# Performance work log

Measured on AMD Instinct MI355X. Metric: run time of the kernel, lower is better.

## Reference

```python
import jax, jax.numpy as jnp
import numpy as np

NUM_SYMBOLS = 5
NUM_SUBCARRIERS = 33


def _dft_matrix(n):
    # Unitary DFT matrix: F[j,k] = exp(-2i*pi*j*k/n) / sqrt(n)
    omega = np.exp(-2j * np.pi / n)
    j, k = np.meshgrid(np.arange(n), np.arange(n))
    return (np.power(omega, j * k) / np.sqrt(n)).astype(np.complex64)


def setup_inputs() -> dict:
    key = jax.random.key(0)
    k1, k2 = jax.random.split(key)
    shape = (4096, NUM_SYMBOLS, 4, 4, NUM_SUBCARRIERS)  # (N, S, TXH, TXW, W)
    x_real = jax.random.normal(k1, shape, dtype=jnp.float32)
    x_imag = jax.random.normal(k2, shape, dtype=jnp.float32)
    F_sym = _dft_matrix(NUM_SYMBOLS)
    F_sub = _dft_matrix(NUM_SUBCARRIERS)
    return {
        "x_real": x_real,
        "x_imag": x_imag,
        "F_sym_real": jnp.asarray(F_sym.real, dtype=jnp.float32),
        "F_sym_imag": jnp.asarray(F_sym.imag, dtype=jnp.float32),
        "F_sub_real": jnp.asarray(F_sub.real, dtype=jnp.float32),
        "F_sub_imag": jnp.asarray(F_sub.imag, dtype=jnp.float32),
    }


def reference(x_real, x_imag, F_sym_real, F_sym_imag, F_sub_real, F_sub_imag):
    N, S, TXH, TXW, W = x_real.shape
    x = jax.lax.complex(x_real, x_imag).reshape(N, S, TXH * TXW, W)
    x = jnp.transpose(x, (0, 2, 1, 3))  # (N, A, S, W), A = TXH*TXW

    F_sym = jax.lax.complex(F_sym_real, F_sym_imag)  # (S, S)
    F_sub = jax.lax.complex(F_sub_real, F_sub_imag)  # (W, W)

    # 2D DFT across symbols (left) and subcarriers (right)
    X = jnp.einsum("st,natw->nasw", F_sym, x)
    X = jnp.einsum("nasw,wv->nasv", X, F_sub)

    # magnitude-square (power spectrum)
    X_mag_sq = (X.real * X.real + X.imag * X.imag).astype(jnp.complex64)

    # inverse 2D DFT (conjugate transposes) -> autocorrelation
    X = jnp.einsum("st,natw->nasw", F_sym.conj().T, X_mag_sq)
    X = jnp.einsum("nasw,wv->nasv", X, F_sub.conj().T)

    X = jnp.transpose(X, (0, 2, 1, 3))  # (N, S, A, W)
    return X.reshape(N, S, TXH, TXW, W)
```

## Files before the change

### kernel.cpp

```cpp
#include <hip/hip_runtime.h>

#define NS 5
#define NW 33
#define NA 16
#define SW 165
#define BUFS 99
#define CW 11
#define CH (CW*NS)
#define CE (CH*MPW)
#define MPW 5
#define GM 20
#define TPM 11
#define CPT 3
#define THREADS 256

typedef float f2 __attribute__((ext_vector_type(2)));

__device__ __forceinline__ void cmac(f2& z, f2 x, f2 f) {
    asm("v_pk_fma_f32 %0, %1, %2, %0 op_sel:[0,0,0] op_sel_hi:[1,0,1]"
        : "+v"(z) : "v"(x), "v"(f));
    asm("v_pk_fma_f32 %0, %1, %2, %0 op_sel:[1,1,0] op_sel_hi:[0,1,1] neg_lo:[1,0,0]"
        : "+v"(z) : "v"(x), "v"(f));
}

__device__ __forceinline__ void cmacr(f2& z, f2 f, f2 Pp) {
    asm("v_pk_fma_f32 %0, %1, %2, %0 op_sel:[0,0,0] op_sel_hi:[1,1,1] neg_hi:[1,0,0]"
        : "+v"(z) : "v"(f), "v"(Pp));
}

__device__ __forceinline__ void pkfma(f2& z, f2 a, f2 b) {
    asm("v_pk_fma_f32 %0, %1, %2, %0 op_sel:[0,0,0] op_sel_hi:[1,1,1]"
        : "+v"(z) : "v"(a), "v"(b));
}

#define STAGE_LOAD(R, W0)                                                  \
    _Pragma("unroll")                                                      \
    for (int i = 0; i < 5; ++i) {                                          \
        const int e = lane + i * 64;                                       \
        f2 v = (f2){0.f, 0.f};                                             \
        if (e < CE) {                                                      \
            const int gq = e / CH, rq = e - gq * CH;                       \
            const int tq = rq / CW, wq = rq - tq * CW;                     \
            const int Mq = Mw + gq;                                        \
            if (Mq < NM) {                                                 \
                const int nq = Mq >> 4, aq = Mq & 15;                      \
                const int go = ((nq * NS + tq) * NA + aq) * NW + (W0) + wq;\
                v = (f2){x_real[go], x_imag[go]};                          \
            }                                                              \
        }                                                                  \
        R[i] = v;                                                          \
    }

#define STAGE_WRITE(R)                                                     \
    _Pragma("unroll")                                                      \
    for (int i = 0; i < 5; ++i) {                                          \
        const int e = lane + i * 64;                                       \
        if (e < CE) {                                                      \
            const int gq = e / CH, rq = e - gq * CH;                       \
            const int tq = rq / CW, wq = rq - tq * CW;                     \
            wbuf[gq * BUFS + wq * NS + tq] = R[i];                         \
        }                                                                  \
    }

#define COMPUTE_CHUNK(W0)                                                  \
    if (act) {                                                             \
        const f2* bp = wbuf + gg * BUFS;                                   \
        _Pragma("unroll 3")                                                \
        for (int w = 0; w < CW; ++w) {                                     \
            f2 xc[NS];                                                     \
            _Pragma("unroll")                                              \
            for (int t = 0; t < NS; ++t) xc[t] = bp[w * NS + t];           \
            f2 fv[CPT];                                                    \
            _Pragma("unroll")                                              \
            for (int k = 0; k < CPT; ++k)                                  \
                fv[k] = sFsub[((W0) + w) * NW + c0 + k];                   \
            _Pragma("unroll")                                              \
            for (int t = 0; t < NS; ++t)                                   \
                _Pragma("unroll")                                          \
                for (int k = 0; k < CPT; ++k)                              \
                    cmac(V[t][k], xc[t], fv[k]);                           \
        }                                                                  \
    }

__global__ __launch_bounds__(THREADS, 6) void autocorr_kernel(
    const float* __restrict__ x_real, const float* __restrict__ x_imag,
    const float* __restrict__ Fsym_re, const float* __restrict__ Fsym_im,
    const float* __restrict__ Fsub_re, const float* __restrict__ Fsub_im,
    float* __restrict__ out, int NM, int write_complex)
{
    __shared__ f2 sFsym[NS * NS];
    __shared__ f2 sFsub[NW * NW];
    __shared__ f2 buf[GM * BUFS];

    const int tid = threadIdx.x;
    const int wave = tid >> 6;
    const int lane = tid & 63;
    const int Mw = blockIdx.x * GM + wave * MPW;
    f2* const wbuf = &buf[wave * MPW * BUFS];

    for (int i = tid; i < NW * NW; i += THREADS)
        sFsub[i] = (f2){Fsub_re[i], Fsub_im[i]};
    if (tid < NS * NS) sFsym[tid] = (f2){Fsym_re[tid], Fsym_im[tid]};

    f2 rA[5], rB[5];
    STAGE_LOAD(rA, 0);
    STAGE_WRITE(rA);
    __syncthreads();

    STAGE_LOAD(rB, CW);

    const int g = lane / TPM;
    const int j = lane - g * TPM;
    const bool act = (lane < MPW * TPM);
    const int gg = act ? g : 0;
    const int M = Mw + gg;
    const int Ms = (M < NM) ? M : 0;
    const int n = Ms >> 4, a = Ms & 15;
    const int c0 = 3 * j;

    f2 V[NS][CPT];
#pragma unroll
    for (int t = 0; t < NS; ++t)
#pragma unroll
        for (int k = 0; k < CPT; ++k) V[t][k] = (f2){0.f, 0.f};

    COMPUTE_CHUNK(0);
    STAGE_WRITE(rB);
    STAGE_LOAD(rA, 2 * CW);
    asm volatile("s_waitcnt lgkmcnt(0)" ::: "memory");
    COMPUTE_CHUNK(CW);
    STAGE_WRITE(rA);
    asm volatile("s_waitcnt lgkmcnt(0)" ::: "memory");
    COMPUTE_CHUNK(2 * CW);

    f2 T2[3][CPT];
#pragma unroll
    for (int p = 0; p < 3; ++p)
#pragma unroll
        for (int k = 0; k < CPT; ++k) T2[p][k] = (f2){0.f, 0.f};
    if (act) {
#pragma unroll
        for (int s = 0; s < NS; ++s) {
            f2 X[CPT];
#pragma unroll
            for (int k = 0; k < CPT; ++k) X[k] = (f2){0.f, 0.f};
#pragma unroll
            for (int t = 0; t < NS; ++t) {
                f2 f = sFsym[s * NS + t];
#pragma unroll
                for (int k = 0; k < CPT; ++k)
                    cmac(X[k], f, V[t][k]);
            }
#pragma unroll
            for (int k = 0; k < CPT; ++k) {
                const float Pv = X[k].x * X[k].x + X[k].y * X[k].y;
                const f2 Pp = (f2){Pv, Pv};
#pragma unroll
                for (int p = 0; p < 3; ++p)
                    cmacr(T2[p][k], sFsym[s * NS + p], Pp);
            }
        }
        f2* const wb = wbuf + gg * BUFS;
#pragma unroll
        for (int k = 0; k < CPT; ++k)
#pragma unroll
            for (int p = 0; p < 3; ++p)
                wb[(c0 + k) * 3 + p] = T2[p][k];
    }
    asm volatile("s_waitcnt lgkmcnt(0)" ::: "memory");

    if (act) {
        const f2* bp = wbuf + gg * BUFS;
        if (!write_complex) {
            f2 Ypk[3][CPT];
#pragma unroll
            for (int p = 0; p < 3; ++p)
#pragma unroll
                for (int k = 0; k < CPT; ++k) Ypk[p][k] = (f2){0.f, 0.f};
#pragma unroll 3
            for (int v = 0; v < NW; ++v) {
                f2 tc[3];
#pragma unroll
                for (int p = 0; p < 3; ++p) tc[p] = bp[v * 3 + p];
                f2 fw[CPT];
#pragma unroll
                for (int k = 0; k < CPT; ++k) fw[k] = sFsub[(c0 + k) * NW + v];
#pragma unroll
                for (int p = 0; p < 3; ++p)
#pragma unroll
                    for (int k = 0; k < CPT; ++k)
                        pkfma(Ypk[p][k], tc[p], fw[k]);
            }
            if (M < NM) {
                int obase = ((n * NS) * NA + a) * NW;
#pragma unroll
                for (int p = 0; p < 3; ++p) {
                    const int pp = (NS - p) % NS;
#pragma unroll
                    for (int k = 0; k < CPT; ++k) {
                        const int q = c0 + k;
                        const int qq = (NW - q) % NW;
                        const float Yr = Ypk[p][k].x + Ypk[p][k].y;
                        out[obase + p * (NA * NW) + q] = Yr;
                        out[obase + pp * (NA * NW) + qq] = Yr;
                    }
                }
            }
        } else {
            f2 Y[3][CPT];
#pragma unroll
            for (int p = 0; p < 3; ++p)
#pragma unroll
                for (int k = 0; k < CPT; ++k) Y[p][k] = (f2){0.f, 0.f};
            for (int v = 0; v < NW; ++v) {
                f2 tc[3];
#pragma unroll
                for (int p = 0; p < 3; ++p) tc[p] = bp[v * 3 + p];
                f2 fw[CPT];
#pragma unroll
                for (int k = 0; k < CPT; ++k) fw[k] = sFsub[(c0 + k) * NW + v];
#pragma unroll
                for (int p = 0; p < 3; ++p)
#pragma unroll
                    for (int k = 0; k < CPT; ++k) {
                        Y[p][k].x = fmaf(tc[p].x, fw[k].x, Y[p][k].x);
                        Y[p][k].x = fmaf(tc[p].y, fw[k].y, Y[p][k].x);
                        Y[p][k].y = fmaf(tc[p].y, fw[k].x, Y[p][k].y);
                        Y[p][k].y = fmaf(-tc[p].x, fw[k].y, Y[p][k].y);
                    }
            }
            if (M < NM) {
#pragma unroll
                for (int p = 0; p < 3; ++p) {
                    const int pp = (NS - p) % NS;
#pragma unroll
                    for (int k = 0; k < CPT; ++k) {
                        const int q = c0 + k;
                        const int qq = (NW - q) % NW;
                        ((float2*)out)[((n * NS + p) * NA + a) * NW + q] =
                            make_float2(Y[p][k].x, Y[p][k].y);
                        ((float2*)out)[((n * NS + pp) * NA + a) * NW + qq] =
                            make_float2(Y[p][k].x, -Y[p][k].y);
                    }
                }
            }
        }
    }
}

extern "C" void kernel_launch(void* const* d_in, const int* in_sizes, int n_in,
                              void* d_out, int out_size, void* d_ws, size_t ws_size,
                              hipStream_t stream) {
    const float* x_real  = (const float*)d_in[0];
    const float* x_imag  = (const float*)d_in[1];
    const float* Fsym_re = (const float*)d_in[2];
    const float* Fsym_im = (const float*)d_in[3];
    const float* Fsub_re = (const float*)d_in[4];
    const float* Fsub_im = (const float*)d_in[5];

    const int NM = in_sizes[0] / SW;
    const long long n_cplx = (long long)in_sizes[0];
    const int write_complex = ((long long)out_size >= 2 * n_cplx) ? 1 : 0;

    const int blocks = (NM + GM - 1) / GM;

    autocorr_kernel<<<blocks, THREADS, 0, stream>>>(
        x_real, x_imag, Fsym_re, Fsym_im, Fsub_re, Fsub_im,
        (float*)d_out, NM, write_complex);
}
```

Baseline: 191.2 us.

## Replace three-chunk register-prefetch pipeline with two larger unpipelined staging chunks

The input staging over subcarriers drops from three 11-wide chunks, software-pipelined through registers, to two chunks of 19 and 14 columns. Each chunk is loaded and written to LDS straight away, with no prefetch overlapping compute. This cuts the number of stage/compute phases and the registers held for in-flight prefetch, but gives up overlap between global loads and compute. The n/a index computation also moves into the output branches.

```diff
diff --git a/kernel.cpp b/kernel.cpp
--- a/kernel.cpp
+++ b/kernel.cpp
@@ -5,15 +5,21 @@
 #define NA 16
 #define SW 165
 #define BUFS 99
-#define CW 11
-#define CH (CW*NS)
-#define CE (CH*MPW)
 #define MPW 5
 #define GM 20
 #define TPM 11
 #define CPT 3
 #define THREADS 256
 
+#define CW0 19
+#define CH0 (CW0*NS)
+#define CE0 (CH0*MPW)
+#define IT0 8
+#define CW1 14
+#define CH1 (CW1*NS)
+#define CE1 (CH1*MPW)
+#define IT1 6
+
 typedef float f2 __attribute__((ext_vector_type(2)));
 
 __device__ __forceinline__ void cmac(f2& z, f2 x, f2 f) {
@@ -33,40 +39,41 @@
         : "+v"(z) : "v"(a), "v"(b));
 }
 
-#define STAGE_LOAD(R, W0)                                                  \
-    _Pragma("unroll")                                                      \
-    for (int i = 0; i < 5; ++i) {                                          \
-        const int e = lane + i * 64;                                       \
-        f2 v = (f2){0.f, 0.f};                                             \
-        if (e < CE) {                                                      \
-            const int gq = e / CH, rq = e - gq * CH;                       \
-            const int tq = rq / CW, wq = rq - tq * CW;                     \
-            const int Mq = Mw + gq;                                        \
-            if (Mq < NM) {                                                 \
-                const int nq = Mq >> 4, aq = Mq & 15;                      \
-                const int go = ((nq * NS + tq) * NA + aq) * NW + (W0) + wq;\
-                v = (f2){x_real[go], x_imag[go]};                          \
+#define STAGE(CW, CH, CE, NIT, W0)                                         \
+    {                                                                      \
+        f2 rr[NIT];                                                        \
+        _Pragma("unroll")                                                  \
+        for (int i = 0; i < NIT; ++i) {                                    \
+            const int e = lane + i * 64;                                   \
+            f2 v = (f2){0.f, 0.f};                                         \
+            if (e < (CE)) {                                                \
+                const int gq = e / (CH), rq = e - gq * (CH);               \
+                const int tq = rq / (CW), wq = rq - tq * (CW);             \
+                const int Mq = Mw + gq;                                    \
+                if (Mq < NM) {                                             \
+                    const int nq = Mq >> 4, aq = Mq & 15;                  \
+                    const int go = ((nq * NS + tq) * NA + aq) * NW + (W0) + wq; \
+                    v = (f2){x_real[go], x_imag[go]};                      \
+                }                                                          \
+            }                                                              \
+            rr[i] = v;                                                     \
+        }                                                                  \
+        _Pragma("unroll")                                                  \
+        for (int i = 0; i < NIT; ++i) {                                    \
+            const int e = lane + i * 64;                                   \
+            if (e < (CE)) {                                                \
+                const int gq = e / (CH), rq = e - gq * (CH);               \
+                const int tq = rq / (CW), wq = rq - tq * (CW);             \
+                wbuf[gq * BUFS + wq * NS + tq] = rr[i];                    \
             }                                                              \
         }                                                                  \
-        R[i] = v;                                                          \
-    }
-
-#define STAGE_WRITE(R)                                                     \
-    _Pragma("unroll")                                                      \
-    for (int i = 0; i < 5; ++i) {                                          \
-        const int e = lane + i * 64;                                       \
-        if (e < CE) {                                                      \
-            const int gq = e / CH, rq = e - gq * CH;                       \
-            const int tq = rq / CW, wq = rq - tq * CW;                     \
-            wbuf[gq * BUFS + wq * NS + tq] = R[i];                         \
-        }                                                                  \
-    }
-
-#define COMPUTE_CHUNK(W0)                                                  \
+    }
+
+#define COMPUTE_CHUNK(CW, W0)                                              \
     if (act) {                                                             \
         const f2* bp = wbuf + gg * BUFS;                                   \
         _Pragma("unroll 3")                                                \
-        for (int w = 0; w < CW; ++w) {                                     \
+        for (int w = 0; w < (CW); ++w) {                                   \
             f2 xc[NS];                                                     \
             _Pragma("unroll")                                              \
             for (int t = 0; t < NS; ++t) xc[t] = bp[w * NS + t];           \
@@ -102,20 +109,14 @@
         sFsub[i] = (f2){Fsub_re[i], Fsub_im[i]};
     if (tid < NS * NS) sFsym[tid] = (f2){Fsym_re[tid], Fsym_im[tid]};
 
-    f2 rA[5], rB[5];
-    STAGE_LOAD(rA, 0);
-    STAGE_WRITE(rA);
+    STAGE(CW0, CH0, CE0, IT0, 0);
     __syncthreads();
-
-    STAGE_LOAD(rB, CW);
 
     const int g = lane / TPM;
     const int j = lane - g * TPM;
     const bool act = (lane < MPW * TPM);
     const int gg = act ? g : 0;
     const int M = Mw + gg;
-    const int Ms = (M < NM) ? M : 0;
-    const int n = Ms >> 4, a = Ms & 15;
     const int c0 = 3 * j;
 
     f2 V[NS][CPT];
@@ -124,14 +125,12 @@
 #pragma unroll
         for (int k = 0; k < CPT; ++k) V[t][k] = (f2){0.f, 0.f};
 
-    COMPUTE_CHUNK(0);
-    STAGE_WRITE(rB);
-    STAGE_LOAD(rA, 2 * CW);
+    COMPUTE_CHUNK(CW0, 0);
+
+    STAGE(CW1, CH1, CE1, IT1, CW0);
     asm volatile("s_waitcnt lgkmcnt(0)" ::: "memory");
-    COMPUTE_CHUNK(CW);
-    STAGE_WRITE(rA);
-    asm volatile("s_waitcnt lgkmcnt(0)" ::: "memory");
-    COMPUTE_CHUNK(2 * CW);
+
+    COMPUTE_CHUNK(CW1, CW0);
 
     f2 T2[3][CPT];
 #pragma unroll
@@ -192,7 +191,8 @@
                         pkfma(Ypk[p][k], tc[p], fw[k]);
             }
             if (M < NM) {
-                int obase = ((n * NS) * NA + a) * NW;
+                const int n = M >> 4, a = M & 15;
+                const int obase = ((n * NS) * NA + a) * NW;
 #pragma unroll
                 for (int p = 0; p < 3; ++p) {
                     const int pp = (NS - p) % NS;
@@ -230,6 +230,7 @@
                     }
             }
             if (M < NM) {
+                const int n = M >> 4, a = M & 15;
 #pragma unroll
                 for (int p = 0; p < 3; ++p) {
                     const int pp = (NS - p) % NS;
```

Result: faster. 179.6 us (-6.1%).
